# Kernel optimization log

Measured on AMD Instinct MI355X. Metric: run time of the kernel, lower is better.

## Reference

```python
import jax, jax.numpy as jnp
import numpy as np

OUT_NPOINT = 1024
NSAMPLE = 64
RADIUS = 0.32
BN_EPS = 1e-5


def _fps_single(pts, npoint):
    # pts: [N,3] -> indices [npoint], sequential furthest point sampling (starts at index 0,
    # matching pointnet2's furthest_point_sample with dists initialized to 1e10).
    N = pts.shape[0]

    def step(carry, _):
        mind, last = carry
        d = jnp.sum((pts - pts[last]) ** 2, axis=-1)  # [N]
        mind = jnp.minimum(mind, d)
        nxt = jnp.argmax(mind).astype(jnp.int32)
        return (mind, nxt), last

    init = (jnp.full((N,), 1e10, dtype=pts.dtype), jnp.int32(0))
    (_, _), idxs = jax.lax.scan(step, init, None, length=npoint)
    return idxs  # [npoint]


def _ball_query(xyz, new_xyz, radius, nsample):
    # xyz: [B,N,3], new_xyz: [B,M,3] -> idx [B,M,nsample] (first nsample in-ball points,
    # padded with the first found index, matching pointnet2 ball_query semantics).
    N = xyz.shape[1]
    d2 = jnp.sum((new_xyz[:, :, None, :] - xyz[:, None, :, :]) ** 2, axis=-1)  # [B,M,N]
    inball = d2 < radius * radius
    key = jnp.where(inball, jnp.arange(N, dtype=jnp.int32)[None, None, :], jnp.int32(N))
    sorted_keys = jnp.sort(key, axis=-1)[..., :nsample]  # [B,M,nsample]
    valid = sorted_keys < N
    first = jnp.where(sorted_keys[..., 0:1] < N, sorted_keys[..., 0:1], 0)
    return jnp.where(valid, sorted_keys, first)


def _group(features, idx):
    # features: [B,C,N], idx: [B,M,S] -> [B,C,M,S]
    return jax.vmap(lambda f, i: f[:, i])(features, idx)


def setup_inputs() -> dict:
    key = jax.random.key(0)
    ks = jax.random.split(key, 8)
    B, N, Cin, Cout = 8, 4096, 128, 256
    xyz = jax.random.uniform(ks[0], (B, N, 3), dtype=jnp.float32)
    features = jax.random.normal(ks[1], (B, Cin, N), dtype=jnp.float32)
    W = jax.random.normal(ks[2], (Cout, Cin), dtype=jnp.float32) * 0.05  # 1x1 conv weight
    b = jax.random.normal(ks[3], (Cout,), dtype=jnp.float32) * 0.05
    gamma = jax.random.uniform(ks[4], (Cout,), minval=0.5, maxval=1.5, dtype=jnp.float32)
    beta = jax.random.normal(ks[5], (Cout,), dtype=jnp.float32) * 0.1
    run_mean = jax.random.normal(ks[6], (Cout,), dtype=jnp.float32) * 0.1
    run_var = jax.random.uniform(ks[7], (Cout,), minval=0.5, maxval=1.5, dtype=jnp.float32)
    return {"xyz": xyz, "features": features, "W": W, "b": b,
            "gamma": gamma, "beta": beta, "run_mean": run_mean, "run_var": run_var}


def reference(xyz, features, W, b, gamma, beta, run_mean, run_var):
    # FPS to pick OUT_NPOINT centers
    fps_idx = jax.vmap(lambda p: _fps_single(p, OUT_NPOINT))(xyz)          # [B,M]
    new_xyz = jnp.take_along_axis(xyz, fps_idx[:, :, None], axis=1)        # [B,M,3]
    # ball-query neighbor indices and gather features (use_xyz=False)
    idx = _ball_query(xyz, new_xyz, RADIUS, NSAMPLE)                        # [B,M,S]
    grouped = _group(features, idx)                                         # [B,Cin,M,S]
    # pointwise conv (1x1) + BN (inference mode) + ReLU
    out = jnp.einsum('oc,bcms->boms', W, grouped) + b[None, :, None, None]  # [B,Cout,M,S]
    inv = jax.lax.rsqrt(run_var + BN_EPS)
    out = (out - run_mean[None, :, None, None]) * (gamma * inv)[None, :, None, None] + beta[None, :, None, None]
    out = jax.nn.relu(out)
    # max-pool over the neighbor axis
    return jnp.max(out, axis=-1)  # [B,Cout,M]
```

## Files before the change

kernel.cpp:

```cpp
#include <hip/hip_runtime.h>

#define N_PTS 4096
#define B_SZ  8
#define M_OUT 1024
#define NS    64
#define CIN   128
#define COUT  256

typedef float v2f __attribute__((ext_vector_type(2)));

__device__ __forceinline__ float dpp_max_f32(float v) {
  int x = __builtin_bit_cast(int, v);
#define STG(C)                                                              \
  {                                                                         \
    int y = __builtin_amdgcn_update_dpp(x, x, C, 0xF, 0xF, false);          \
    float a = __builtin_bit_cast(float, x);                                 \
    float b2 = __builtin_bit_cast(float, y);                                \
    a = fmaxf(a, b2);                                                       \
    x = __builtin_bit_cast(int, a);                                         \
  }
  STG(0x111) STG(0x112) STG(0x114) STG(0x118) STG(0x142) STG(0x143)
#undef STG
  return __builtin_bit_cast(float, __builtin_amdgcn_readlane(x, 63));
}

__global__ __launch_bounds__(256) void fps_conv_kernel(
    const float* __restrict__ xyz, int* __restrict__ fps_idx,
    const float* __restrict__ F, const float* __restrict__ W,
    float* __restrict__ Z) {
  __shared__ __align__(16) float smem[13360];
  if (blockIdx.x < 8) {
#pragma clang fp contract(off)
    float* lx = smem;
    float* ly = smem + 4096;
    float* lz = smem + 8192;
    float4 (*sl)[4] = (float4(*)[4])(smem + 12288);
    int (*siw)[4] = (int(*)[4])(smem + 12320);
    int* wlds = (int*)(smem + 12328);
    const int b = blockIdx.x, t = threadIdx.x;
    const int lane = t & 63, wv = t >> 6;
    const float* base = xyz + b * N_PTS * 3;
    for (int e = t; e < N_PTS; e += 256) {
      lx[e] = base[e * 3 + 0];
      ly[e] = base[e * 3 + 1];
      lz[e] = base[e * 3 + 2];
    }
    __syncthreads();
    const int nb = t * 16;
    v2f px[8], py[8], pz[8], m2[8];
#pragma unroll
    for (int j = 0; j < 8; ++j) {
      int n0 = nb + 2 * j;
      px[j] = (v2f){lx[n0], lx[n0 + 1]};
      py[j] = (v2f){ly[n0], ly[n0 + 1]};
      pz[j] = (v2f){lz[n0], lz[n0 + 1]};
      m2[j] = (v2f){1e10f, 1e10f};
    }
    int cur = 0;
    float cx = lx[0], cy = ly[0], cz = lz[0];
    for (int i = 0; i < M_OUT; ++i) {
      if (t == 0) wlds[i] = cur;
      float bv = -1.0f;
      int bj = 0;
#pragma unroll
      for (int j = 0; j < 8; ++j) {
        v2f dx = px[j] - cx, dy = py[j] - cy, dz = pz[j] - cz;
        v2f d = dx * dx + dy * dy;
        d = d + dz * dz;
        v2f md = __builtin_elementwise_min(m2[j], d);
        m2[j] = md;
        if (md.x > bv) { bv = md.x; bj = 2 * j; }
        if (md.y > bv) { bv = md.y; bj = 2 * j + 1; }
      }
      const float mv = dpp_max_f32(bv);
      unsigned long long tied = __ballot(bv == mv);
      const int fl = __ffsll(tied) - 1;
      const int bi = nb + bj;
      const int widx = __builtin_amdgcn_readlane(bi, fl);
      const float wx = lx[widx], wy = ly[widx], wz = lz[widx];
      const int p = i & 1;
      if (lane == 0) {
        sl[p][wv] = make_float4(mv, wx, wy, wz);
        siw[p][wv] = widx;
      }
      __syncthreads();
      float4 s0 = sl[p][0], s1 = sl[p][1], s2 = sl[p][2], s3 = sl[p][3];
      int i0 = siw[p][0], i1 = siw[p][1], i2 = siw[p][2], i3 = siw[p][3];
      float gv = s0.x, gx = s0.y, gy = s0.z, gz = s0.w;
      int gi = i0;
      bool bt;
      bt = (s1.x > gv) || (s1.x == gv && i1 < gi);
      if (bt) { gv = s1.x; gi = i1; gx = s1.y; gy = s1.z; gz = s1.w; }
      bt = (s2.x > gv) || (s2.x == gv && i2 < gi);
      if (bt) { gv = s2.x; gi = i2; gx = s2.y; gy = s2.z; gz = s2.w; }
      bt = (s3.x > gv) || (s3.x == gv && i3 < gi);
      if (bt) { gv = s3.x; gi = i3; gx = s3.y; gy = s3.z; gz = s3.w; }
      cur = gi; cx = gx; cy = gy; cz = gz;
    }
    __syncthreads();
    for (int e = t; e < M_OUT; e += 256) fps_idx[b * M_OUT + e] = wlds[e];
  } else {
    float (*Bs)[68] = (float(*)[68])smem;
    float (*As)[68] = (float(*)[68])(smem + 8704);
    const int bid = blockIdx.x - 8;
    const int n0 = (bid & 63) * 64;
    const int o0 = ((bid >> 6) & 3) * 64;
    const int b = bid >> 8;
    const int tid = threadIdx.x;
    for (int l = 0; l < 32; ++l) {
      int e = l * 256 + tid;
      int c = e & 127, oo = e >> 7;
      Bs[c][oo] = W[(o0 + oo) * CIN + c];
    }
    float acc[4][4] = {};
    const int tx = tid & 15, ty = tid >> 4;
    const float* Fb = F + b * CIN * N_PTS;
    for (int c0 = 0; c0 < CIN; c0 += 32) {
      __syncthreads();
      for (int l = 0; l < 8; ++l) {
        int e = l * 256 + tid;
        int nn = e & 63, cc = e >> 6;
        As[cc][nn] = Fb[(c0 + cc) * N_PTS + n0 + nn];
      }
      __syncthreads();
#pragma unroll
      for (int cc = 0; cc < 32; ++cc) {
        float4 a = *(const float4*)&As[cc][tx * 4];
        float4 w4 = *(const float4*)&Bs[c0 + cc][ty * 4];
        acc[0][0] += a.x * w4.x; acc[0][1] += a.x * w4.y; acc[0][2] += a.x * w4.z; acc[0][3] += a.x * w4.w;
        acc[1][0] += a.y * w4.x; acc[1][1] += a.y * w4.y; acc[1][2] += a.y * w4.z; acc[1][3] += a.y * w4.w;
        acc[2][0] += a.z * w4.x; acc[2][1] += a.z * w4.y; acc[2][2] += a.z * w4.z; acc[2][3] += a.z * w4.w;
        acc[3][0] += a.w * w4.x; acc[3][1] += a.w * w4.y; acc[3][2] += a.w * w4.z; acc[3][3] += a.w * w4.w;
      }
    }
    float* Zb = Z + (size_t)(b * N_PTS + n0) * COUT + o0;
#pragma unroll
    for (int i = 0; i < 4; ++i) {
      int nn = tx * 4 + i;
      float4 v = make_float4(acc[i][0], acc[i][1], acc[i][2], acc[i][3]);
      *(float4*)&Zb[(size_t)nn * COUT + ty * 4] = v;
    }
  }
}

__global__ __launch_bounds__(256) void ballq_pool_kernel(
    const float* __restrict__ xyz, const int* __restrict__ fps_idx,
    const float* __restrict__ Z, const float* __restrict__ bias,
    const float* __restrict__ gamma, const float* __restrict__ beta,
    const float* __restrict__ rmean, const float* __restrict__ rvar,
    float* __restrict__ out) {
  __shared__ float T[COUT][9];
  __shared__ __align__(16) int sidx[8 * NS];
  const int b = blockIdx.x & 7;
  const int m0 = (blockIdx.x >> 3) * 8;
  const int lane = threadIdx.x & 63, wv = threadIdx.x >> 6;
  const float* base = xyz + b * N_PTS * 3;
  {
#pragma clang fp contract(off)
    for (int cc2 = 0; cc2 < 2; ++cc2) {
      const int c = 2 * wv + cc2;
      const int cidx = fps_idx[b * M_OUT + m0 + c];
      const float cx = base[cidx * 3 + 0], cy = base[cidx * 3 + 1],
                  cz = base[cidx * 3 + 2];
      int* srow = sidx + c * NS;
      int cnt = 0, first = 0;
      for (int ch = 0; ch < N_PTS / 64 && cnt < NS; ++ch) {
        const int n = ch * 64 + lane;
        float dx = base[n * 3 + 0] - cx;
        float dy = base[n * 3 + 1] - cy;
        float dz = base[n * 3 + 2] - cz;
        float d = dx * dx + dy * dy;
        d = d + dz * dz;
        const bool inb = d < 0.1024f;
        unsigned long long mask = __ballot(inb);
        if (cnt == 0 && mask) first = ch * 64 + (__ffsll(mask) - 1);
        const int pos = cnt + __popcll(mask & ((1ull << lane) - 1ull));
        if (inb && pos < NS) srow[pos] = n;
        cnt += (int)__popcll(mask);
      }
      if (lane >= cnt) srow[lane] = first;
    }
  }
  __syncthreads();
  const int o = threadIdx.x;
  const float sc = gamma[o] * (1.0f / sqrtf(rvar[o] + 1e-5f));
  const float bo = bias[o], mo = rmean[o], bt = beta[o];
  const float* Zb = Z + (size_t)b * N_PTS * COUT;
  for (int mi = 0; mi < 8; ++mi) {
    float b0 = -1e30f, b1 = -1e30f, b2 = -1e30f, b3 = -1e30f;
#pragma unroll
    for (int s = 0; s < NS; s += 4) {
      int4 iv = *(const int4*)&sidx[mi * NS + s];
      b0 = fmaxf(b0, Zb[(size_t)iv.x * COUT + o]);
      b1 = fmaxf(b1, Zb[(size_t)iv.y * COUT + o]);
      b2 = fmaxf(b2, Zb[(size_t)iv.z * COUT + o]);
      b3 = fmaxf(b3, Zb[(size_t)iv.w * COUT + o]);
    }
    float best = fmaxf(fmaxf(b0, b1), fmaxf(b2, b3));
    float t = best + bo;
    t = (t - mo) * sc + bt;
    T[o][mi] = fmaxf(t, 0.0f);
  }
  __syncthreads();
  for (int l = 0; l < 8; ++l) {
    int e = l * 256 + (int)threadIdx.x;
    int mm = e & 7, oo = e >> 3;
    out[(size_t)(b * COUT + oo) * M_OUT + m0 + mm] = T[oo][mm];
  }
}

extern "C" void kernel_launch(void* const* d_in, const int* in_sizes, int n_in,
                              void* d_out, int out_size, void* d_ws, size_t ws_size,
                              hipStream_t stream) {
  const float* xyz      = (const float*)d_in[0];
  const float* features = (const float*)d_in[1];
  const float* W        = (const float*)d_in[2];
  const float* bias     = (const float*)d_in[3];
  const float* gamma    = (const float*)d_in[4];
  const float* beta     = (const float*)d_in[5];
  const float* rmean    = (const float*)d_in[6];
  const float* rvar     = (const float*)d_in[7];
  float* out = (float*)d_out;

  char* ws = (char*)d_ws;
  int* fps  = (int*)ws;
  float* Z  = (float*)(ws + (64 << 10) + (2 << 20));

  fps_conv_kernel<<<8 + 2048, 256, 0, stream>>>(xyz, fps, features, W, Z);
  ballq_pool_kernel<<<B_SZ * (M_OUT / 8), 256, 0, stream>>>(
      xyz, fps, Z, bias, gamma, beta, rmean, rvar, out);
}
```

Measured before the change: 849.2 us.

## Fuse ball-query pooling into FPS/conv kernel with per-batch progress flags

Merges the ball-query/max-pool stage into the FPS+conv launch. FPS blocks publish their progress every 16 centers through global atomic counters, and conv blocks count completed tiles per batch. Pool blocks, each now handling 32 centers instead of 8, spin-wait on these flags, so pooling can overlap the tail of the sequential FPS and the separate kernel launch disappears. This relies on the FPS and conv blocks being scheduled before the spinning pool blocks; otherwise it could deadlock. It also adds a memset and spin-polling overhead.

```diff
diff --git a/kernel.cpp b/kernel.cpp
--- a/kernel.cpp
+++ b/kernel.cpp
@@ -24,10 +24,13 @@
   return __builtin_bit_cast(float, __builtin_amdgcn_readlane(x, 63));
 }
 
-__global__ __launch_bounds__(256) void fps_conv_kernel(
+__global__ __launch_bounds__(256) void fps_conv_pool_kernel(
     const float* __restrict__ xyz, int* __restrict__ fps_idx,
     const float* __restrict__ F, const float* __restrict__ W,
-    float* __restrict__ Z) {
+    float* __restrict__ Z, int* __restrict__ sync,
+    const float* __restrict__ bias, const float* __restrict__ gamma,
+    const float* __restrict__ beta, const float* __restrict__ rmean,
+    const float* __restrict__ rvar, float* __restrict__ out) {
   __shared__ __align__(16) float smem[13360];
   if (blockIdx.x < 8) {
 #pragma clang fp contract(off)
@@ -36,10 +39,10 @@
     float* lz = smem + 8192;
     float4 (*sl)[4] = (float4(*)[4])(smem + 12288);
     int (*siw)[4] = (int(*)[4])(smem + 12320);
-    int* wlds = (int*)(smem + 12328);
     const int b = blockIdx.x, t = threadIdx.x;
     const int lane = t & 63, wv = t >> 6;
     const float* base = xyz + b * N_PTS * 3;
+    int* fout = fps_idx + b * M_OUT;
     for (int e = t; e < N_PTS; e += 256) {
       lx[e] = base[e * 3 + 0];
       ly[e] = base[e * 3 + 1];
@@ -59,7 +62,14 @@
     int cur = 0;
     float cx = lx[0], cy = ly[0], cz = lz[0];
     for (int i = 0; i < M_OUT; ++i) {
-      if (t == 0) wlds[i] = cur;
+      if (t == 0) {
+        fout[i] = cur;
+        if ((i & 15) == 15) {
+          __threadfence();
+          __hip_atomic_store(&sync[b], i + 1, __ATOMIC_RELEASE,
+                             __HIP_MEMORY_SCOPE_AGENT);
+        }
+      }
       float bv = -1.0f;
       int bj = 0;
 #pragma unroll
@@ -97,9 +107,7 @@
       if (bt) { gv = s3.x; gi = i3; gx = s3.y; gy = s3.z; gz = s3.w; }
       cur = gi; cx = gx; cy = gy; cz = gz;
     }
-    __syncthreads();
-    for (int e = t; e < M_OUT; e += 256) fps_idx[b * M_OUT + e] = wlds[e];
-  } else {
+  } else if (blockIdx.x < 2056) {
     float (*Bs)[68] = (float(*)[68])smem;
     float (*As)[68] = (float(*)[68])(smem + 8704);
     const int bid = blockIdx.x - 8;
@@ -140,72 +148,82 @@
       float4 v = make_float4(acc[i][0], acc[i][1], acc[i][2], acc[i][3]);
       *(float4*)&Zb[(size_t)nn * COUT + ty * 4] = v;
     }
-  }
-}
-
-__global__ __launch_bounds__(256) void ballq_pool_kernel(
-    const float* __restrict__ xyz, const int* __restrict__ fps_idx,
-    const float* __restrict__ Z, const float* __restrict__ bias,
-    const float* __restrict__ gamma, const float* __restrict__ beta,
-    const float* __restrict__ rmean, const float* __restrict__ rvar,
-    float* __restrict__ out) {
-  __shared__ float T[COUT][9];
-  __shared__ __align__(16) int sidx[8 * NS];
-  const int b = blockIdx.x & 7;
-  const int m0 = (blockIdx.x >> 3) * 8;
-  const int lane = threadIdx.x & 63, wv = threadIdx.x >> 6;
-  const float* base = xyz + b * N_PTS * 3;
-  {
+    __syncthreads();
+    if (tid == 0) {
+      __threadfence();
+      __hip_atomic_fetch_add(&sync[8 + b], 1, __ATOMIC_RELEASE,
+                             __HIP_MEMORY_SCOPE_AGENT);
+    }
+  } else {
+    float (*T)[33] = (float(*)[33])smem;
+    int* sidx = (int*)(smem + 8448);
+    const int pid = blockIdx.x - 2056;
+    const int b = pid & 7;
+    const int m0 = (pid >> 3) * 32;
+    const int lane = threadIdx.x & 63, wv = threadIdx.x >> 6;
+    if (threadIdx.x == 0) {
+      while (__hip_atomic_load(&sync[b], __ATOMIC_ACQUIRE,
+                               __HIP_MEMORY_SCOPE_AGENT) < m0 + 32)
+        __builtin_amdgcn_s_sleep(2);
+      while (__hip_atomic_load(&sync[8 + b], __ATOMIC_ACQUIRE,
+                               __HIP_MEMORY_SCOPE_AGENT) < 256)
+        __builtin_amdgcn_s_sleep(2);
+      __threadfence();
+    }
+    __syncthreads();
+    const float* base = xyz + b * N_PTS * 3;
+    {
 #pragma clang fp contract(off)
-    for (int cc2 = 0; cc2 < 2; ++cc2) {
-      const int c = 2 * wv + cc2;
-      const int cidx = fps_idx[b * M_OUT + m0 + c];
-      const float cx = base[cidx * 3 + 0], cy = base[cidx * 3 + 1],
-                  cz = base[cidx * 3 + 2];
-      int* srow = sidx + c * NS;
-      int cnt = 0, first = 0;
-      for (int ch = 0; ch < N_PTS / 64 && cnt < NS; ++ch) {
-        const int n = ch * 64 + lane;
-        float dx = base[n * 3 + 0] - cx;
-        float dy = base[n * 3 + 1] - cy;
-        float dz = base[n * 3 + 2] - cz;
-        float d = dx * dx + dy * dy;
-        d = d + dz * dz;
-        const bool inb = d < 0.1024f;
-        unsigned long long mask = __ballot(inb);
-        if (cnt == 0 && mask) first = ch * 64 + (__ffsll(mask) - 1);
-        const int pos = cnt + __popcll(mask & ((1ull << lane) - 1ull));
-        if (inb && pos < NS) srow[pos] = n;
-        cnt += (int)__popcll(mask);
-      }
-      if (lane >= cnt) srow[lane] = first;
-    }
-  }
-  __syncthreads();
-  const int o = threadIdx.x;
-  const float sc = gamma[o] * (1.0f / sqrtf(rvar[o] + 1e-5f));
-  const float bo = bias[o], mo = rmean[o], bt = beta[o];
-  const float* Zb = Z + (size_t)b * N_PTS * COUT;
-  for (int mi = 0; mi < 8; ++mi) {
-    float b0 = -1e30f, b1 = -1e30f, b2 = -1e30f, b3 = -1e30f;
-#pragma unroll
-    for (int s = 0; s < NS; s += 4) {
-      int4 iv = *(const int4*)&sidx[mi * NS + s];
-      b0 = fmaxf(b0, Zb[(size_t)iv.x * COUT + o]);
-      b1 = fmaxf(b1, Zb[(size_t)iv.y * COUT + o]);
-      b2 = fmaxf(b2, Zb[(size_t)iv.z * COUT + o]);
-      b3 = fmaxf(b3, Zb[(size_t)iv.w * COUT + o]);
-    }
-    float best = fmaxf(fmaxf(b0, b1), fmaxf(b2, b3));
-    float t = best + bo;
-    t = (t - mo) * sc + bt;
-    T[o][mi] = fmaxf(t, 0.0f);
-  }
-  __syncthreads();
-  for (int l = 0; l < 8; ++l) {
-    int e = l * 256 + (int)threadIdx.x;
-    int mm = e & 7, oo = e >> 3;
-    out[(size_t)(b * COUT + oo) * M_OUT + m0 + mm] = T[oo][mm];
+      for (int cc2 = 0; cc2 < 8; ++cc2) {
+        const int c = 8 * wv + cc2;
+        const int cidx = fps_idx[b * M_OUT + m0 + c];
+        const float cx = base[cidx * 3 + 0], cy = base[cidx * 3 + 1],
+                    cz = base[cidx * 3 + 2];
+        int* srow = sidx + c * NS;
+        int cnt = 0, first = 0;
+        for (int ch = 0; ch < N_PTS / 64 && cnt < NS; ++ch) {
+          const int n = ch * 64 + lane;
+          float dx = base[n * 3 + 0] - cx;
+          float dy = base[n * 3 + 1] - cy;
+          float dz = base[n * 3 + 2] - cz;
+          float d = dx * dx + dy * dy;
+          d = d + dz * dz;
+          const bool inb = d < 0.1024f;
+          unsigned long long mask = __ballot(inb);
+          if (cnt == 0 && mask) first = ch * 64 + (__ffsll(mask) - 1);
+          const int pos = cnt + __popcll(mask & ((1ull << lane) - 1ull));
+          if (inb && pos < NS) srow[pos] = n;
+          cnt += (int)__popcll(mask);
+        }
+        if (lane >= cnt) srow[lane] = first;
+      }
+    }
+    __syncthreads();
+    const int o = threadIdx.x;
+    const float sc = gamma[o] * (1.0f / sqrtf(rvar[o] + 1e-5f));
+    const float bo = bias[o], mo = rmean[o], bt = beta[o];
+    const float* Zb = Z + (size_t)b * N_PTS * COUT;
+    for (int mi = 0; mi < 32; ++mi) {
+      float b0 = -1e30f, b1 = -1e30f, b2 = -1e30f, b3 = -1e30f;
+#pragma unroll
+      for (int s = 0; s < NS; s += 4) {
+        int4 iv = *(const int4*)&sidx[mi * NS + s];
+        b0 = fmaxf(b0, Zb[(size_t)iv.x * COUT + o]);
+        b1 = fmaxf(b1, Zb[(size_t)iv.y * COUT + o]);
+        b2 = fmaxf(b2, Zb[(size_t)iv.z * COUT + o]);
+        b3 = fmaxf(b3, Zb[(size_t)iv.w * COUT + o]);
+      }
+      float best = fmaxf(fmaxf(b0, b1), fmaxf(b2, b3));
+      float t = best + bo;
+      t = (t - mo) * sc + bt;
+      T[o][mi] = fmaxf(t, 0.0f);
+    }
+    __syncthreads();
+    for (int l = 0; l < 32; ++l) {
+      int e = l * 256 + (int)threadIdx.x;
+      int mm = e & 31, oo = e >> 5;
+      out[(size_t)(b * COUT + oo) * M_OUT + m0 + mm] = T[oo][mm];
+    }
   }
 }
 
@@ -223,10 +241,11 @@
   float* out = (float*)d_out;
 
   char* ws = (char*)d_ws;
-  int* fps  = (int*)ws;
-  float* Z  = (float*)(ws + (64 << 10) + (2 << 20));
-
-  fps_conv_kernel<<<8 + 2048, 256, 0, stream>>>(xyz, fps, features, W, Z);
-  ballq_pool_kernel<<<B_SZ * (M_OUT / 8), 256, 0, stream>>>(
-      xyz, fps, Z, bias, gamma, beta, rmean, rvar, out);
+  int* fps   = (int*)ws;
+  int* syncp = (int*)(ws + 32768);
+  float* Z   = (float*)(ws + (64 << 10) + (2 << 20));
+
+  hipMemsetAsync(syncp, 0, 64, stream);
+  fps_conv_pool_kernel<<<8 + 2048 + 256, 256, 0, stream>>>(
+      xyz, fps, features, W, Z, syncp, bias, gamma, beta, rmean, rvar, out);
 }
```

Measured after the change: 972.5 us. 1.15x slower.

## Run FPS in a single wavefront to drop per-iteration block barrier

Applied to the files above, without the earlier changes.

FPS now runs in one 64-lane wavefront per batch, with each lane holding 64 points in registers. This removes the per-iteration LDS exchange, the __syncthreads, and the cross-wave merge, since the DPP reduction and ballot already pick the global argmax. Indices are written straight to global memory, and launch bounds now hint one block per CU. The cost is 4x more serial arithmetic per lane on only one SIMD, plus higher register pressure that could affect the conv blocks in the same kernel.

```diff
diff --git a/kernel.cpp b/kernel.cpp
--- a/kernel.cpp
+++ b/kernel.cpp
@@ -24,7 +24,7 @@
   return __builtin_bit_cast(float, __builtin_amdgcn_readlane(x, 63));
 }
 
-__global__ __launch_bounds__(256) void fps_conv_kernel(
+__global__ __launch_bounds__(256, 1) void fps_conv_kernel(
     const float* __restrict__ xyz, int* __restrict__ fps_idx,
     const float* __restrict__ F, const float* __restrict__ W,
     float* __restrict__ Z) {
@@ -34,11 +34,7 @@
     float* lx = smem;
     float* ly = smem + 4096;
     float* lz = smem + 8192;
-    float4 (*sl)[4] = (float4(*)[4])(smem + 12288);
-    int (*siw)[4] = (int(*)[4])(smem + 12320);
-    int* wlds = (int*)(smem + 12328);
     const int b = blockIdx.x, t = threadIdx.x;
-    const int lane = t & 63, wv = t >> 6;
     const float* base = xyz + b * N_PTS * 3;
     for (int e = t; e < N_PTS; e += 256) {
       lx[e] = base[e * 3 + 0];
@@ -46,10 +42,11 @@
       lz[e] = base[e * 3 + 2];
     }
     __syncthreads();
-    const int nb = t * 16;
-    v2f px[8], py[8], pz[8], m2[8];
-#pragma unroll
-    for (int j = 0; j < 8; ++j) {
+    if (t >= 64) return;
+    const int nb = t * 64;
+    v2f px[32], py[32], pz[32], m2[32];
+#pragma unroll
+    for (int j = 0; j < 32; ++j) {
       int n0 = nb + 2 * j;
       px[j] = (v2f){lx[n0], lx[n0 + 1]};
       py[j] = (v2f){ly[n0], ly[n0 + 1]};
@@ -58,12 +55,13 @@
     }
     int cur = 0;
     float cx = lx[0], cy = ly[0], cz = lz[0];
+    int* fout = fps_idx + b * M_OUT;
     for (int i = 0; i < M_OUT; ++i) {
-      if (t == 0) wlds[i] = cur;
+      if (t == 0) fout[i] = cur;
       float bv = -1.0f;
       int bj = 0;
 #pragma unroll
-      for (int j = 0; j < 8; ++j) {
+      for (int j = 0; j < 32; ++j) {
         v2f dx = px[j] - cx, dy = py[j] - cy, dz = pz[j] - cz;
         v2f d = dx * dx + dy * dy;
         d = d + dz * dz;
@@ -77,28 +75,9 @@
       const int fl = __ffsll(tied) - 1;
       const int bi = nb + bj;
       const int widx = __builtin_amdgcn_readlane(bi, fl);
-      const float wx = lx[widx], wy = ly[widx], wz = lz[widx];
-      const int p = i & 1;
-      if (lane == 0) {
-        sl[p][wv] = make_float4(mv, wx, wy, wz);
-        siw[p][wv] = widx;
-      }
-      __syncthreads();
-      float4 s0 = sl[p][0], s1 = sl[p][1], s2 = sl[p][2], s3 = sl[p][3];
-      int i0 = siw[p][0], i1 = siw[p][1], i2 = siw[p][2], i3 = siw[p][3];
-      float gv = s0.x, gx = s0.y, gy = s0.z, gz = s0.w;
-      int gi = i0;
-      bool bt;
-      bt = (s1.x > gv) || (s1.x == gv && i1 < gi);
-      if (bt) { gv = s1.x; gi = i1; gx = s1.y; gy = s1.z; gz = s1.w; }
-      bt = (s2.x > gv) || (s2.x == gv && i2 < gi);
-      if (bt) { gv = s2.x; gi = i2; gx = s2.y; gy = s2.z; gz = s2.w; }
-      bt = (s3.x > gv) || (s3.x == gv && i3 < gi);
-      if (bt) { gv = s3.x; gi = i3; gx = s3.y; gy = s3.z; gz = s3.w; }
-      cur = gi; cx = gx; cy = gy; cz = gz;
-    }
-    __syncthreads();
-    for (int e = t; e < M_OUT; e += 256) fps_idx[b * M_OUT + e] = wlds[e];
+      cx = lx[widx]; cy = ly[widx]; cz = lz[widx];
+      cur = widx;
+    }
   } else {
     float (*Bs)[68] = (float(*)[68])smem;
     float (*As)[68] = (float(*)[68])(smem + 8704);
```

Measured after the change: 1.628 ms. 1.92x slower.
